# Kernel tuning notes

Hardware: AMD Instinct MI355X
Metric: run time of the kernel (lower is better)

## Reference

```python
import jax, jax.numpy as jnp
import numpy as np

BL = 5
N = 2 ** BL  # 32; LUT is (N+1) x (N+1)


def setup_inputs() -> dict:
    key = jax.random.key(0)
    k1, k2, k3 = jax.random.split(key, 3)
    M, K, O = 512, 256, 256
    x = jax.random.uniform(k1, (M, K), dtype=jnp.float32)              # activations in [0,1)
    W = jax.random.uniform(k2, (O, K), dtype=jnp.float32) * 2.0 - 1.0  # weights in [-1,1)
    b = jax.random.uniform(k3, (O,), dtype=jnp.float32) * 2.0 - 1.0
    # Stochastic-computing multiplication LUT: A[i, j] ~ i*j/N (floored), i,j in [0, N]
    i = np.arange(N + 1, dtype=np.float32)
    lut = jnp.asarray(np.floor(np.outer(i, i) / N), dtype=jnp.float32)
    return {"x": x, "W": W, "b": b, "lut": lut}


def _sanitize(t):
    t = jnp.where(jnp.isnan(t), jnp.zeros_like(t), t)
    return jnp.where(jnp.isinf(t), jnp.ones_like(t), t)


def sc_mat_mac_p(a, b, c, lut, n):
    # Faithful port of SC_MAT_MAC_p: quantize -> LUT gather over all (row, out) pairs ->
    # sign-correct -> reduce over K -> requantize -> add quantized bias -> rescale.
    a = _sanitize(a)
    b = _sanitize(b)
    c = _sanitize(c)
    amax = jnp.abs(a).max()
    amax = jnp.where(amax == 0, jnp.ones_like(amax), amax)
    dmax = jnp.maximum(jnp.abs(b).max(), jnp.abs(c).max())
    dmax = jnp.where(dmax == 0, jnp.ones_like(dmax), dmax)
    # SBL2 = int(log2(int(N / amax))); SN2 = 2**SBL2 (truncations match torch int())
    sn2 = 2.0 ** jnp.floor(jnp.log2(jnp.floor(n / amax)))
    sn1 = 2.0 ** jnp.floor(jnp.log2(jnp.floor(n / dmax)))
    aa = (a * sn2).astype(jnp.int32)  # [M, K], |aa| <= N
    bb = (b * sn1).astype(jnp.int32)  # [O, K], |bb| <= N
    cc = (c * sn1).astype(jnp.int32)  # [O]
    # LUT gather over the full cross product (original materializes this via
    # repeat_interleave/repeat; here it is a broadcasted gather of shape [M, O, K]).
    prod = lut[jnp.abs(aa)[:, None, :], jnp.abs(bb)[None, :, :]]          # [M, O, K]
    sgn = (jnp.sign(aa)[:, None, :] * jnp.sign(bb)[None, :, :]).astype(prod.dtype)
    x9 = (sgn * prod).sum(axis=-1)                                        # [M, O]
    d = (x9 / sn2).astype(jnp.int32) + cc[None, :]
    return d.astype(jnp.float32) / sn1


def reference(x, W, b, lut):
    # out = linear(x); out.data = SC_MAT_MAC_p(...)  -> value is the SC result,
    # gradient path is the dense linear (straight-through via .data assignment).
    lin = x @ W.T + b
    p = sc_mat_mac_p(x, W, b, lut, N)
    return lin + jax.lax.stop_gradient(p - lin)
```

## Files before the change

kernel.cpp:

```cpp
#include <hip/hip_runtime.h>
#include <stdint.h>


#define MROWS 512
#define KDIM  256
#define OCOLS 256
#define RB    64

__device__ __forceinline__ void get_scales(float amax, float dmax, int& e2, int& e1) {
    if (amax == 0.0f) amax = 1.0f;
    if (dmax == 0.0f) dmax = 1.0f;
    float q2 = 32.0f / amax;
    float q1 = 32.0f / dmax;
    int f2 = (q2 >= 1073741824.0f) ? 0x40000000 : (int)floorf(q2);
    int f1 = (q1 >= 1073741824.0f) ? 0x40000000 : (int)floorf(q1);
    if (f2 < 1) f2 = 1;
    if (f1 < 1) f1 = 1;
    e2 = 31 - __clz(f2);
    e1 = 31 - __clz(f1);
}

__global__ __launch_bounds__(256)
void k_reduce(const float* __restrict__ x, const float* __restrict__ W,
              const float* __restrict__ b, float* __restrict__ wsp) {
    __shared__ float sm[8];
    const int g = blockIdx.x * 256 + threadIdx.x;
    const float4* xf = (const float4*)x;
    const float4* wf = (const float4*)W;
    const float4* bf = (const float4*)b;

    float4 x0 = xf[g];
    float4 x1 = xf[g + 16384];
    float4 wv = wf[g];
    float va = fmaxf(fmaxf(fabsf(x0.x), fabsf(x0.y)), fmaxf(fabsf(x0.z), fabsf(x0.w)));
    va = fmaxf(va, fmaxf(fmaxf(fabsf(x1.x), fabsf(x1.y)), fmaxf(fabsf(x1.z), fabsf(x1.w))));
    float vd = fmaxf(fmaxf(fabsf(wv.x), fabsf(wv.y)), fmaxf(fabsf(wv.z), fabsf(wv.w)));
    if (g < 64) {
        float4 bv = bf[g];
        vd = fmaxf(vd, fmaxf(fmaxf(fabsf(bv.x), fabsf(bv.y)), fmaxf(fabsf(bv.z), fabsf(bv.w))));
    }
    #pragma unroll
    for (int m = 32; m >= 1; m >>= 1) {
        va = fmaxf(va, __shfl_xor(va, m, 64));
        vd = fmaxf(vd, __shfl_xor(vd, m, 64));
    }
    const int wv_id = threadIdx.x >> 6;
    if ((threadIdx.x & 63) == 0) { sm[2 * wv_id] = va; sm[2 * wv_id + 1] = vd; }
    __syncthreads();
    if (threadIdx.x == 0) {
        float a = fmaxf(fmaxf(sm[0], sm[2]), fmaxf(sm[4], sm[6]));
        float d = fmaxf(fmaxf(sm[1], sm[3]), fmaxf(sm[5], sm[7]));
        wsp[2 * blockIdx.x]     = a;
        wsp[2 * blockIdx.x + 1] = d;
    }
}

__global__ __launch_bounds__(256)
void k_main(const float* __restrict__ wsp, const float* __restrict__ x,
            const float* __restrict__ W, const float* __restrict__ b,
            float* __restrict__ out) {
    __shared__ unsigned int a_sh[KDIM / 4];
    __shared__ float s_max[2];

    const int m = blockIdx.x;
    const int o = threadIdx.x;

    if (o < 64) {
        float va = wsp[2 * o];
        float vd = wsp[2 * o + 1];
        #pragma unroll
        for (int s = 32; s >= 1; s >>= 1) {
            va = fmaxf(va, __shfl_xor(va, s, 64));
            vd = fmaxf(vd, __shfl_xor(vd, s, 64));
        }
        if (o == 0) { s_max[0] = va; s_max[1] = vd; }
    }
    __syncthreads();

    int e2, e1;
    get_scales(s_max[0], s_max[1], e2, e1);
    const float sn2f = (float)(1 << e2);
    const float sn1f = (float)(1 << e1);

    if (o < KDIM / 4) {
        float4 xv = ((const float4*)(x + (size_t)m * KDIM))[o];
        int a0 = (int)(xv.x * sn2f) & 0xFF;
        int a1 = (int)(xv.y * sn2f) & 0xFF;
        int a2 = (int)(xv.z * sn2f) & 0xFF;
        int a3 = (int)(xv.w * sn2f) & 0xFF;
        a_sh[o] = (unsigned int)(a0 | (a1 << 8) | (a2 << 16) | (a3 << 24));
    }
    __syncthreads();

    const float4* wrow = (const float4*)(W + (size_t)o * KDIM);
    int sum = 0;
    #pragma unroll 8
    for (int kk = 0; kk < KDIM / 4; ++kk) {
        float4 wv = wrow[kk];
        unsigned int ap = a_sh[kk];
        float wfv[4] = {wv.x, wv.y, wv.z, wv.w};
        #pragma unroll
        for (int j = 0; j < 4; ++j) {
            int bv = (int)(wfv[j] * sn1f);
            int av = ((int)(ap << (24 - 8 * j))) >> 24;
            int s  = av * bv;
            sum += (s + ((s >> 31) & 31)) >> 5;
        }
    }

    int cc = (int)(b[o] * sn1f);
    int d  = ((sum + ((sum >> 31) & ((1 << e2) - 1))) >> e2) + cc;
    out[(size_t)m * OCOLS + o] = (float)d / sn1f;
}

extern "C" void kernel_launch(void* const* d_in, const int* in_sizes, int n_in,
                              void* d_out, int out_size, void* d_ws, size_t ws_size,
                              hipStream_t stream) {
    const float* x = (const float*)d_in[0];
    const float* W = (const float*)d_in[1];
    const float* b = (const float*)d_in[2];
    float* out = (float*)d_out;
    float* wsp = (float*)d_ws;

    k_reduce<<<RB, 256, 0, stream>>>(x, W, b, wsp);
    k_main<<<MROWS, 256, 0, stream>>>(wsp, x, W, b, out);
}
```

Measured before the change: 77.70 us.

## Fuse max-reduction and main kernel via cooperative grid sync

Merges the two-kernel pipeline into one cooperative kernel. Each of the 512 blocks first computes a partial abs-max over a slice of x, W and b, then the blocks meet at a grid-wide sync, and every block reduces the 512 partials before running the LUT-style MAC. This removes one kernel launch and the gap between launches, but adds a grid barrier and a cooperative-launch requirement that all 512 blocks be resident at once.

```diff
diff --git a/kernel.cpp b/kernel.cpp
--- a/kernel.cpp
+++ b/kernel.cpp
@@ -1,11 +1,13 @@
 #include <hip/hip_runtime.h>
+#include <hip/hip_cooperative_groups.h>
 #include <stdint.h>
+
+namespace cg = cooperative_groups;
 
 
 #define MROWS 512
 #define KDIM  256
 #define OCOLS 256
-#define RB    64
 
 __device__ __forceinline__ void get_scales(float amax, float dmax, int& e2, int& e1) {
     if (amax == 0.0f) amax = 1.0f;
@@ -20,62 +22,63 @@
     e1 = 31 - __clz(f1);
 }
 
-__global__ __launch_bounds__(256)
-void k_reduce(const float* __restrict__ x, const float* __restrict__ W,
-              const float* __restrict__ b, float* __restrict__ wsp) {
-    __shared__ float sm[8];
-    const int g = blockIdx.x * 256 + threadIdx.x;
-    const float4* xf = (const float4*)x;
-    const float4* wf = (const float4*)W;
-    const float4* bf = (const float4*)b;
-
-    float4 x0 = xf[g];
-    float4 x1 = xf[g + 16384];
-    float4 wv = wf[g];
-    float va = fmaxf(fmaxf(fabsf(x0.x), fabsf(x0.y)), fmaxf(fabsf(x0.z), fabsf(x0.w)));
-    va = fmaxf(va, fmaxf(fmaxf(fabsf(x1.x), fabsf(x1.y)), fmaxf(fabsf(x1.z), fabsf(x1.w))));
-    float vd = fmaxf(fmaxf(fabsf(wv.x), fabsf(wv.y)), fmaxf(fabsf(wv.z), fabsf(wv.w)));
-    if (g < 64) {
-        float4 bv = bf[g];
-        vd = fmaxf(vd, fmaxf(fmaxf(fabsf(bv.x), fabsf(bv.y)), fmaxf(fabsf(bv.z), fabsf(bv.w))));
-    }
-    #pragma unroll
-    for (int m = 32; m >= 1; m >>= 1) {
-        va = fmaxf(va, __shfl_xor(va, m, 64));
-        vd = fmaxf(vd, __shfl_xor(vd, m, 64));
-    }
-    const int wv_id = threadIdx.x >> 6;
-    if ((threadIdx.x & 63) == 0) { sm[2 * wv_id] = va; sm[2 * wv_id + 1] = vd; }
-    __syncthreads();
-    if (threadIdx.x == 0) {
-        float a = fmaxf(fmaxf(sm[0], sm[2]), fmaxf(sm[4], sm[6]));
-        float d = fmaxf(fmaxf(sm[1], sm[3]), fmaxf(sm[5], sm[7]));
-        wsp[2 * blockIdx.x]     = a;
-        wsp[2 * blockIdx.x + 1] = d;
-    }
+__device__ __forceinline__ float max4(float4 v) {
+    return fmaxf(fmaxf(fabsf(v.x), fabsf(v.y)), fmaxf(fabsf(v.z), fabsf(v.w)));
 }
 
 __global__ __launch_bounds__(256)
-void k_main(const float* __restrict__ wsp, const float* __restrict__ x,
-            const float* __restrict__ W, const float* __restrict__ b,
-            float* __restrict__ out) {
+void k_fused(float* __restrict__ wsp, const float* __restrict__ x,
+             const float* __restrict__ W, const float* __restrict__ b,
+             float* __restrict__ out) {
     __shared__ unsigned int a_sh[KDIM / 4];
+    __shared__ float sm[8];
     __shared__ float s_max[2];
 
     const int m = blockIdx.x;
     const int o = threadIdx.x;
+    const int wave = o >> 6;
 
-    if (o < 64) {
-        float va = wsp[2 * o];
-        float vd = wsp[2 * o + 1];
+    {
+        const int g = m * 256 + o;
+        float va = 0.0f, vd = 0.0f;
+        if (g < 32768) {
+            va = max4(((const float4*)x)[g]);
+        } else if (g < 49152) {
+            vd = max4(((const float4*)W)[g - 32768]);
+        } else if (g < 49216) {
+            vd = max4(((const float4*)b)[g - 49152]);
+        }
         #pragma unroll
         for (int s = 32; s >= 1; s >>= 1) {
             va = fmaxf(va, __shfl_xor(va, s, 64));
             vd = fmaxf(vd, __shfl_xor(vd, s, 64));
         }
-        if (o == 0) { s_max[0] = va; s_max[1] = vd; }
+        if ((o & 63) == 0) { sm[2 * wave] = va; sm[2 * wave + 1] = vd; }
+        __syncthreads();
+        if (o == 0) {
+            wsp[2 * m]     = fmaxf(fmaxf(sm[0], sm[2]), fmaxf(sm[4], sm[6]));
+            wsp[2 * m + 1] = fmaxf(fmaxf(sm[1], sm[3]), fmaxf(sm[5], sm[7]));
+        }
     }
-    __syncthreads();
+
+    cg::this_grid().sync();
+
+    {
+        float va = fmaxf(wsp[2 * o], wsp[2 * (o + 256)]);
+        float vd = fmaxf(wsp[2 * o + 1], wsp[2 * (o + 256) + 1]);
+        #pragma unroll
+        for (int s = 32; s >= 1; s >>= 1) {
+            va = fmaxf(va, __shfl_xor(va, s, 64));
+            vd = fmaxf(vd, __shfl_xor(vd, s, 64));
+        }
+        if ((o & 63) == 0) { sm[2 * wave] = va; sm[2 * wave + 1] = vd; }
+        __syncthreads();
+        if (o == 0) {
+            s_max[0] = fmaxf(fmaxf(sm[0], sm[2]), fmaxf(sm[4], sm[6]));
+            s_max[1] = fmaxf(fmaxf(sm[1], sm[3]), fmaxf(sm[5], sm[7]));
+        }
+        __syncthreads();
+    }
 
     int e2, e1;
     get_scales(s_max[0], s_max[1], e2, e1);
@@ -122,6 +125,7 @@
     float* out = (float*)d_out;
     float* wsp = (float*)d_ws;
 
-    k_reduce<<<RB, 256, 0, stream>>>(x, W, b, wsp);
-    k_main<<<MROWS, 256, 0, stream>>>(wsp, x, W, b, out);
+    void* args[] = { (void*)&wsp, (void*)&x, (void*)&W, (void*)&b, (void*)&out };
+    hipLaunchCooperativeKernel((const void*)k_fused, dim3(MROWS), dim3(256),
+                               args, 0, stream);
 }
```

Result: slower. 125.6 us (+61.7%).
